# Kernel tuning notes

Hardware: AMD Instinct MI355X
Metric: run time of the kernel (lower is better)

The kernel has to match this reference:

```python
import jax, jax.numpy as jnp
import numpy as np

B, NNZ = 2048, 8
CAT_V, HVEC_V = 10000, 50000
SYN, SEM = 128, 256
HIDDEN, OUT = 1024, 10000


def setup_inputs() -> dict:
    key = jax.random.key(0)
    ks = jax.random.split(key, 12)
    d_onehot = jax.nn.one_hot(jax.random.randint(ks[0], (B,), 0, 7), 7, dtype=jnp.float32)
    cat_b_ix = jax.random.randint(ks[1], (B,), 0, CAT_V)
    hvb_ix = jax.random.randint(ks[2], (B, NNZ), 0, HVEC_V)
    hvf_ix = jax.random.randint(ks[3], (B, NNZ), 0, HVEC_V)
    hvb_top = jax.random.normal(ks[4], (B, SEM), dtype=jnp.float32)
    hvf_top = jax.random.normal(ks[5], (B, SEM), dtype=jnp.float32)
    cat_embeds = jax.random.normal(ks[6], (CAT_V, SYN), dtype=jnp.float32) * 0.02
    hvec_embeds = jax.random.normal(ks[7], (HVEC_V, SEM), dtype=jnp.float32) * 0.02
    in_dim = 7 + SYN + 2 * SEM
    W1 = jax.random.normal(ks[8], (HIDDEN, in_dim), dtype=jnp.float32) / np.sqrt(in_dim)
    b1 = jnp.zeros((HIDDEN,), dtype=jnp.float32)
    W2 = jax.random.normal(ks[9], (OUT, HIDDEN), dtype=jnp.float32) / np.sqrt(HIDDEN)
    b2 = jnp.zeros((OUT,), dtype=jnp.float32)
    return {"d_onehot": d_onehot, "cat_b_ix": cat_b_ix, "hvb_ix": hvb_ix,
            "hvf_ix": hvf_ix, "hvb_top": hvb_top, "hvf_top": hvf_top,
            "cat_embeds": cat_embeds, "hvec_embeds": hvec_embeds,
            "W1": W1, "b1": b1, "W2": W2, "b2": b2}


def _multi_hot(ix, vocab):
    # set-to-1 semantics: duplicates within a row still yield 1 (matches torch loop)
    rows = jnp.arange(ix.shape[0])[:, None]
    return jnp.zeros((ix.shape[0], vocab), dtype=jnp.float32).at[rows, ix].set(1.0)


def reference(d_onehot, cat_b_ix, hvb_ix, hvf_ix, hvb_top, hvf_top,
              cat_embeds, hvec_embeds, W1, b1, W2, b2):
    cat_b_embed = cat_embeds[cat_b_ix]                      # (B, SYN)
    hvb_mat = _multi_hot(hvb_ix, hvec_embeds.shape[0])      # (B, HVEC_V)
    hvf_mat = _multi_hot(hvf_ix, hvec_embeds.shape[0])
    hvb_embed = hvb_mat @ hvec_embeds + hvb_top             # (B, SEM)
    hvf_embed = hvf_mat @ hvec_embeds + hvf_top
    x = jnp.concatenate([cat_b_embed, hvb_embed, hvf_embed, d_onehot], axis=1)
    x = jax.nn.relu(x @ W1.T + b1)
    x = x @ W2.T + b2
    return jax.nn.log_softmax(x, axis=1)
```

## Files before the change

kernel.cpp:

```cpp
#include <hip/hip_runtime.h>

#define B_      2048
#define SYN     128
#define SEM     256
#define IN_DIM  647
#define K1      704
#define HIDDEN  1024
#define OUT_N   10000
#define NNZ     8

typedef __bf16 bf16x8 __attribute__((ext_vector_type(8)));
typedef float  f32x4  __attribute__((ext_vector_type(4)));
typedef __attribute__((address_space(3))) const unsigned short* lds_cp;

__device__ __forceinline__ unsigned short f2b(float v) {
    __bf16 b = (__bf16)v;
    return __builtin_bit_cast(unsigned short, b);
}
__device__ __forceinline__ float b2f(unsigned short u) {
    unsigned v = ((unsigned)u) << 16;
    return __builtin_bit_cast(float, v);
}

__global__ __launch_bounds__(256) void build_x(
    const float* __restrict__ d_onehot,
    const int*   __restrict__ cat_ix,
    const int*   __restrict__ hvb_ix,
    const int*   __restrict__ hvf_ix,
    const float* __restrict__ hvb_top,
    const float* __restrict__ hvf_top,
    const float* __restrict__ cat_embeds,
    const float* __restrict__ hvec_embeds,
    unsigned short* __restrict__ xb)
{
    const int b = blockIdx.x, t = threadIdx.x;
    unsigned short* xrow = xb + (size_t)b * K1;

    if (t < SYN) {
        int c = cat_ix[b];
        xrow[t] = f2b(cat_embeds[(size_t)c * SYN + t]);
    }
    {
        int ix[NNZ];
        #pragma unroll
        for (int j = 0; j < NNZ; ++j) ix[j] = hvb_ix[b * NNZ + j];
        float s = hvb_top[(size_t)b * SEM + t];
        #pragma unroll
        for (int j = 0; j < NNZ; ++j) {
            bool dup = false;
            for (int k2 = 0; k2 < j; ++k2) dup = dup || (ix[j] == ix[k2]);
            if (!dup) s += hvec_embeds[(size_t)ix[j] * SEM + t];
        }
        xrow[SYN + t] = f2b(s);
    }
    {
        int ix[NNZ];
        #pragma unroll
        for (int j = 0; j < NNZ; ++j) ix[j] = hvf_ix[b * NNZ + j];
        float s = hvf_top[(size_t)b * SEM + t];
        #pragma unroll
        for (int j = 0; j < NNZ; ++j) {
            bool dup = false;
            for (int k2 = 0; k2 < j; ++k2) dup = dup || (ix[j] == ix[k2]);
            if (!dup) s += hvec_embeds[(size_t)ix[j] * SEM + t];
        }
        xrow[SYN + SEM + t] = f2b(s);
    }
    if (t < 7)       xrow[640 + t] = f2b(d_onehot[b * 7 + t]);
    else if (t < 64) xrow[640 + t] = 0;
}

__global__ void cvt_w1(const float* __restrict__ W1, unsigned short* __restrict__ W1b) {
    int idx = blockIdx.x * 256 + threadIdx.x;
    if (idx >= HIDDEN * K1) return;
    int r = idx / K1, c = idx - r * K1;
    W1b[idx] = f2b(c < IN_DIM ? W1[r * IN_DIM + c] : 0.f);
}

__global__ __launch_bounds__(256) void cvt_w2(const float* __restrict__ W2,
                                              unsigned short* __restrict__ W2b) {
    size_t i = (size_t)blockIdx.x * 256 + threadIdx.x;
    if (i >= (size_t)OUT_N * HIDDEN / 8) return;
    const float4* src = (const float4*)(W2 + i * 8);
    float4 a = src[0], b = src[1];
    ushort u[8] = { f2b(a.x), f2b(a.y), f2b(a.z), f2b(a.w),
                    f2b(b.x), f2b(b.y), f2b(b.z), f2b(b.w) };
    *(uint4*)(W2b + i * 8) = *(const uint4*)u;
}

template<int NI, int MODE>
__global__ __launch_bounds__(256) void gemm_rt(
    const unsigned short* __restrict__ A,
    const unsigned short* __restrict__ Bm,
    const float* __restrict__ bias,
    void* __restrict__ outp,
    int K, int nt, int ncols, int nbm1, int nm)
{
    constexpr int BN    = 32 * NI;
    constexpr int NB_CH = NI / 2;
    __shared__ __align__(16) unsigned short lds_a[4][128 * 32];
    __shared__ __align__(16) unsigned short lds_b[4][BN * 32];

    const int tid = threadIdx.x;
    const int wv = tid >> 6, ln = tid & 63;
    const int wr = wv >> 1, wc = wv & 1;
    const int lr = ln & 15, lh = ln >> 4;

    const int g   = gridDim.x;
    const int nw  = (blockIdx.x & 7) * (g >> 3) + (blockIdx.x >> 3);
    const int mt  = nw % nm, ntile = nw / nm;
    const int m0  = mt * 128, n0 = ntile * BN;

    const unsigned short* srcA[2];
    const unsigned short* srcB[NB_CH];
    #pragma unroll
    for (int i = 0; i < 2; ++i) {
        int c = tid + i * 256;
        int row = c >> 2, colL = (((c & 3) ^ ((c >> 3) & 3)) << 3);
        srcA[i] = A + (size_t)(m0 + row) * K + colL;
    }
    #pragma unroll
    for (int j = 0; j < NB_CH; ++j) {
        int c = tid + j * 256;
        int row = c >> 2, colL = (((c & 3) ^ ((c >> 3) & 3)) << 3);
        int gr = n0 + row; if (gr > nbm1) gr = nbm1;
        srcB[j] = Bm + (size_t)gr * K + colL;
    }

    auto stage = [&](int buf, int kt) {
        #pragma unroll
        for (int i = 0; i < 2; ++i)
            __builtin_amdgcn_global_load_lds(
                (__attribute__((address_space(1))) const void*)(srcA[i] + kt),
                (__attribute__((address_space(3))) void*)&lds_a[buf][(tid + i * 256) * 8], 16, 0, 0);
        #pragma unroll
        for (int j = 0; j < NB_CH; ++j)
            __builtin_amdgcn_global_load_lds(
                (__attribute__((address_space(1))) const void*)(srcB[j] + kt),
                (__attribute__((address_space(3))) void*)&lds_b[buf][(tid + j * 256) * 8], 16, 0, 0);
    };

    int a_off[4], b_off[NI];
    #pragma unroll
    for (int mi = 0; mi < 4; ++mi) {
        int row = wr * 64 + mi * 16 + lr;
        a_off[mi] = (row * 64 + lh * 16) ^ (((row >> 1) & 3) << 4);
    }
    #pragma unroll
    for (int ni = 0; ni < NI; ++ni) {
        int row = wc * 16 * NI + ni * 16 + lr;
        b_off[ni] = (row * 64 + lh * 16) ^ (((row >> 1) & 3) << 4);
    }

    f32x4 acc[4][NI];
    {
        f32x4 z = {0.f, 0.f, 0.f, 0.f};
        #pragma unroll
        for (int i = 0; i < 4; ++i)
            #pragma unroll
            for (int j = 0; j < NI; ++j) acc[i][j] = z;
    }

    stage(0, 0);
    stage(1, 32);
    if constexpr (NI == 4) asm volatile("s_waitcnt vmcnt(4)" ::: "memory");
    else                   asm volatile("s_waitcnt vmcnt(3)" ::: "memory");
    __builtin_amdgcn_s_barrier();
    asm volatile("" ::: "memory");

    for (int t = 0; t < nt; ++t) {
        const int cur = t & 3, pre = (t + 2) & 3;
        int tp = t + 2; if (tp > nt - 1) tp = nt - 1;

        bf16x8 af[4], bfv[NI];
        lds_cp pa = (lds_cp)&lds_a[cur][0];
        lds_cp pb = (lds_cp)&lds_b[cur][0];
        #pragma unroll
        for (int mi = 0; mi < 4; ++mi) {
            unsigned ad = (unsigned)(unsigned long long)pa + a_off[mi];
            asm volatile("ds_read_b128 %0, %1" : "=v"(af[mi]) : "v"(ad));
        }
        #pragma unroll
        for (int ni = 0; ni < NI; ++ni) {
            unsigned ad = (unsigned)(unsigned long long)pb + b_off[ni];
            asm volatile("ds_read_b128 %0, %1" : "=v"(bfv[ni]) : "v"(ad));
        }

        stage(pre, tp * 32);

        asm volatile("s_waitcnt lgkmcnt(0)" ::: "memory");
        __builtin_amdgcn_sched_barrier(0);

        __builtin_amdgcn_s_setprio(1);
        #pragma unroll
        for (int mi = 0; mi < 4; ++mi)
            #pragma unroll
            for (int ni = 0; ni < NI; ++ni)
                acc[mi][ni] = __builtin_amdgcn_mfma_f32_16x16x32_bf16(af[mi], bfv[ni], acc[mi][ni], 0, 0, 0);
        __builtin_amdgcn_s_setprio(0);

        if constexpr (NI == 4) asm volatile("s_waitcnt vmcnt(4)" ::: "memory");
        else                   asm volatile("s_waitcnt vmcnt(3)" ::: "memory");
        __builtin_amdgcn_s_barrier();
        asm volatile("" ::: "memory");
    }

    #pragma unroll
    for (int mi = 0; mi < 4; ++mi) {
        int row = m0 + wr * 64 + mi * 16 + lh * 4;
        #pragma unroll
        for (int ni = 0; ni < NI; ++ni) {
            int col = n0 + wc * 16 * NI + ni * 16 + lr;
            if (col < ncols) {
                float bb = bias[col];
                if (MODE == 0) {
                    unsigned short* H = (unsigned short*)outp;
                    #pragma unroll
                    for (int r = 0; r < 4; ++r)
                        H[(size_t)(row + r) * ncols + col] = f2b(fmaxf(acc[mi][ni][r] + bb, 0.f));
                } else if (MODE == 1) {
                    unsigned short* H = (unsigned short*)outp;
                    #pragma unroll
                    for (int r = 0; r < 4; ++r)
                        H[(size_t)(row + r) * ncols + col] = f2b(acc[mi][ni][r] + bb);
                } else {
                    float* O = (float*)outp;
                    #pragma unroll
                    for (int r = 0; r < 4; ++r)
                        O[(size_t)(row + r) * ncols + col] = acc[mi][ni][r] + bb;
                }
            }
        }
    }
}

__global__ __launch_bounds__(256) void lsm_b(const unsigned short* __restrict__ lg,
                                             float* __restrict__ out) {
    __shared__ __align__(16) float rowbuf[OUT_N];
    __shared__ float red[8];
    const int t = threadIdx.x, wv = t >> 6, ln = t & 63;
    const unsigned short* l = lg + (size_t)blockIdx.x * OUT_N;
    float* o = out + (size_t)blockIdx.x * OUT_N;

    float mx = -3.4e38f;
    for (int i = t; i < OUT_N / 8; i += 256) {
        uint4 v = ((const uint4*)l)[i];
        float f[8];
        unsigned w[4] = {v.x, v.y, v.z, v.w};
        #pragma unroll
        for (int j = 0; j < 4; ++j) {
            f[2*j]   = __builtin_bit_cast(float, w[j] << 16);
            f[2*j+1] = __builtin_bit_cast(float, w[j] & 0xffff0000u);
        }
        #pragma unroll
        for (int j = 0; j < 8; ++j) {
            rowbuf[i * 8 + j] = f[j];
            mx = fmaxf(mx, f[j]);
        }
    }
    #pragma unroll
    for (int off = 32; off > 0; off >>= 1) mx = fmaxf(mx, __shfl_xor(mx, off, 64));
    if (ln == 0) red[wv] = mx;
    __syncthreads();
    float m4 = fmaxf(fmaxf(red[0], red[1]), fmaxf(red[2], red[3]));

    float s = 0.f;
    for (int i = t; i < OUT_N; i += 256) s += __expf(rowbuf[i] - m4);
    #pragma unroll
    for (int off = 32; off > 0; off >>= 1) s += __shfl_xor(s, off, 64);
    if (ln == 0) red[4 + wv] = s;
    __syncthreads();
    float lz = m4 + logf(red[4] + red[5] + red[6] + red[7]);

    for (int i = t; i < OUT_N / 4; i += 256) {
        float4 v = { rowbuf[i*4] - lz, rowbuf[i*4+1] - lz,
                     rowbuf[i*4+2] - lz, rowbuf[i*4+3] - lz };
        ((float4*)o)[i] = v;
    }
}

__global__ __launch_bounds__(256) void lsm_f(float* __restrict__ out) {
    __shared__ __align__(16) float rowbuf[OUT_N];
    __shared__ float red[8];
    const int t = threadIdx.x, wv = t >> 6, ln = t & 63;
    float* o = out + (size_t)blockIdx.x * OUT_N;

    float mx = -3.4e38f;
    for (int i = t; i < OUT_N / 4; i += 256) {
        float4 v = ((const float4*)o)[i];
        rowbuf[i*4] = v.x; rowbuf[i*4+1] = v.y; rowbuf[i*4+2] = v.z; rowbuf[i*4+3] = v.w;
        mx = fmaxf(fmaxf(mx, fmaxf(v.x, v.y)), fmaxf(v.z, v.w));
    }
    #pragma unroll
    for (int off = 32; off > 0; off >>= 1) mx = fmaxf(mx, __shfl_xor(mx, off, 64));
    if (ln == 0) red[wv] = mx;
    __syncthreads();
    float m4 = fmaxf(fmaxf(red[0], red[1]), fmaxf(red[2], red[3]));

    float s = 0.f;
    for (int i = t; i < OUT_N; i += 256) s += __expf(rowbuf[i] - m4);
    #pragma unroll
    for (int off = 32; off > 0; off >>= 1) s += __shfl_xor(s, off, 64);
    if (ln == 0) red[4 + wv] = s;
    __syncthreads();
    float lz = m4 + logf(red[4] + red[5] + red[6] + red[7]);

    for (int i = t; i < OUT_N / 4; i += 256) {
        float4 v = { rowbuf[i*4] - lz, rowbuf[i*4+1] - lz,
                     rowbuf[i*4+2] - lz, rowbuf[i*4+3] - lz };
        ((float4*)o)[i] = v;
    }
}

extern "C" void kernel_launch(void* const* d_in, const int* in_sizes, int n_in,
                              void* d_out, int out_size, void* d_ws, size_t ws_size,
                              hipStream_t stream) {
    const float* d_onehot    = (const float*)d_in[0];
    const int*   cat_ix      = (const int*)  d_in[1];
    const int*   hvb_ix      = (const int*)  d_in[2];
    const int*   hvf_ix      = (const int*)  d_in[3];
    const float* hvb_top     = (const float*)d_in[4];
    const float* hvf_top     = (const float*)d_in[5];
    const float* cat_embeds  = (const float*)d_in[6];
    const float* hvec_embeds = (const float*)d_in[7];
    const float* W1          = (const float*)d_in[8];
    const float* b1          = (const float*)d_in[9];
    const float* W2          = (const float*)d_in[10];
    const float* b2          = (const float*)d_in[11];
    float* out = (float*)d_out;

    unsigned short* xb  = (unsigned short*)d_ws;
    unsigned short* W1b = xb  + (size_t)B_ * K1;
    unsigned short* hB  = W1b + (size_t)HIDDEN * K1;
    unsigned short* W2b = hB  + (size_t)B_ * HIDDEN;
    unsigned short* lg  = W2b + (size_t)OUT_N * HIDDEN;
    const size_t need = ((size_t)B_*K1 + (size_t)HIDDEN*K1 + (size_t)B_*HIDDEN
                         + (size_t)OUT_N*HIDDEN + (size_t)B_*OUT_N) * 2;
    const bool bf16_logits = (ws_size >= need);

    cvt_w1<<<dim3((HIDDEN * K1 + 255) / 256), dim3(256), 0, stream>>>(W1, W1b);
    cvt_w2<<<dim3((OUT_N * HIDDEN / 8 + 255) / 256), dim3(256), 0, stream>>>(W2, W2b);
    build_x<<<dim3(B_), dim3(256), 0, stream>>>(d_onehot, cat_ix, hvb_ix, hvf_ix,
                                                hvb_top, hvf_top, cat_embeds, hvec_embeds, xb);
    gemm_rt<2, 0><<<dim3(256), dim3(256), 0, stream>>>(
        xb, W1b, b1, (void*)hB, K1, K1 / 32, HIDDEN, HIDDEN - 1, 16);
    if (bf16_logits) {
        gemm_rt<4, 1><<<dim3(16 * 79), dim3(256), 0, stream>>>(
            hB, W2b, b2, (void*)lg, HIDDEN, HIDDEN / 32, OUT_N, OUT_N - 1, 16);
        lsm_b<<<dim3(B_), dim3(256), 0, stream>>>(lg, out);
    } else {
        gemm_rt<4, 2><<<dim3(16 * 79), dim3(256), 0, stream>>>(
            hB, W2b, b2, (void*)out, HIDDEN, HIDDEN / 32, OUT_N, OUT_N - 1, 16);
        lsm_f<<<dim3(B_), dim3(256), 0, stream>>>(out);
    }
}
```

Measured before the change: 119.2 us.

## Fuse prep kernels and double-buffer GEMM fragments with deeper prefetch

Merges the W1/W2 bf16 conversion and input-row building into a single prep launch, removing two kernel launches and gaps. Restructures the GEMM main loop to ping-pong register fragments so LDS reads for the next tile overlap MFMAs of the current one, and prefetches three tiles ahead instead of two. Uses partial lgkmcnt waits; increases register pressure and assumes an even tile count.

New measurement: 116.3 us. 2.5% less time.

```diff
diff --git a/kernel.cpp b/kernel.cpp
--- a/kernel.cpp
+++ b/kernel.cpp
@@ -17,12 +17,12 @@
     __bf16 b = (__bf16)v;
     return __builtin_bit_cast(unsigned short, b);
 }
-__device__ __forceinline__ float b2f(unsigned short u) {
-    unsigned v = ((unsigned)u) << 16;
-    return __builtin_bit_cast(float, v);
-}
-
-__global__ __launch_bounds__(256) void build_x(
+
+#define NB_W1 2816
+#define NB_W2 5000
+__global__ __launch_bounds__(256) void prep(
+    const float* __restrict__ W1,  unsigned short* __restrict__ W1b,
+    const float* __restrict__ W2,  unsigned short* __restrict__ W2b,
     const float* __restrict__ d_onehot,
     const int*   __restrict__ cat_ix,
     const int*   __restrict__ hvb_ix,
@@ -33,9 +33,24 @@
     const float* __restrict__ hvec_embeds,
     unsigned short* __restrict__ xb)
 {
-    const int b = blockIdx.x, t = threadIdx.x;
+    const int bb = blockIdx.x, t = threadIdx.x;
+    if (bb < NB_W1) {
+        int idx = bb * 256 + t;
+        int r = idx / K1, c = idx - r * K1;
+        W1b[idx] = f2b(c < IN_DIM ? W1[r * IN_DIM + c] : 0.f);
+        return;
+    }
+    if (bb < NB_W1 + NB_W2) {
+        size_t i = (size_t)(bb - NB_W1) * 256 + t;
+        const float4* src = (const float4*)(W2 + i * 8);
+        float4 a = src[0], b = src[1];
+        ushort u[8] = { f2b(a.x), f2b(a.y), f2b(a.z), f2b(a.w),
+                        f2b(b.x), f2b(b.y), f2b(b.z), f2b(b.w) };
+        *(uint4*)(W2b + i * 8) = *(const uint4*)u;
+        return;
+    }
+    const int b = bb - (NB_W1 + NB_W2);
     unsigned short* xrow = xb + (size_t)b * K1;
-
     if (t < SYN) {
         int c = cat_ix[b];
         xrow[t] = f2b(cat_embeds[(size_t)c * SYN + t]);
@@ -68,24 +83,6 @@
     }
     if (t < 7)       xrow[640 + t] = f2b(d_onehot[b * 7 + t]);
     else if (t < 64) xrow[640 + t] = 0;
-}
-
-__global__ void cvt_w1(const float* __restrict__ W1, unsigned short* __restrict__ W1b) {
-    int idx = blockIdx.x * 256 + threadIdx.x;
-    if (idx >= HIDDEN * K1) return;
-    int r = idx / K1, c = idx - r * K1;
-    W1b[idx] = f2b(c < IN_DIM ? W1[r * IN_DIM + c] : 0.f);
-}
-
-__global__ __launch_bounds__(256) void cvt_w2(const float* __restrict__ W2,
-                                              unsigned short* __restrict__ W2b) {
-    size_t i = (size_t)blockIdx.x * 256 + threadIdx.x;
-    if (i >= (size_t)OUT_N * HIDDEN / 8) return;
-    const float4* src = (const float4*)(W2 + i * 8);
-    float4 a = src[0], b = src[1];
-    ushort u[8] = { f2b(a.x), f2b(a.y), f2b(a.z), f2b(a.w),
-                    f2b(b.x), f2b(b.y), f2b(b.z), f2b(b.w) };
-    *(uint4*)(W2b + i * 8) = *(const uint4*)u;
 }
 
 template<int NI, int MODE>
@@ -161,20 +158,9 @@
             for (int j = 0; j < NI; ++j) acc[i][j] = z;
     }
 
-    stage(0, 0);
-    stage(1, 32);
-    if constexpr (NI == 4) asm volatile("s_waitcnt vmcnt(4)" ::: "memory");
-    else                   asm volatile("s_waitcnt vmcnt(3)" ::: "memory");
-    __builtin_amdgcn_s_barrier();
-    asm volatile("" ::: "memory");
-
-    for (int t = 0; t < nt; ++t) {
-        const int cur = t & 3, pre = (t + 2) & 3;
-        int tp = t + 2; if (tp > nt - 1) tp = nt - 1;
-
-        bf16x8 af[4], bfv[NI];
-        lds_cp pa = (lds_cp)&lds_a[cur][0];
-        lds_cp pb = (lds_cp)&lds_b[cur][0];
+    auto frag_read = [&](bf16x8 (&af)[4], bf16x8 (&bfv)[NI], int buf) {
+        lds_cp pa = (lds_cp)&lds_a[buf][0];
+        lds_cp pb = (lds_cp)&lds_b[buf][0];
         #pragma unroll
         for (int mi = 0; mi < 4; ++mi) {
             unsigned ad = (unsigned)(unsigned long long)pa + a_off[mi];
@@ -185,24 +171,43 @@
             unsigned ad = (unsigned)(unsigned long long)pb + b_off[ni];
             asm volatile("ds_read_b128 %0, %1" : "=v"(bfv[ni]) : "v"(ad));
         }
-
-        stage(pre, tp * 32);
-
-        asm volatile("s_waitcnt lgkmcnt(0)" ::: "memory");
-        __builtin_amdgcn_sched_barrier(0);
-
-        __builtin_amdgcn_s_setprio(1);
+    };
+    auto do_mfma = [&](bf16x8 (&af)[4], bf16x8 (&bfv)[NI]) {
         #pragma unroll
         for (int mi = 0; mi < 4; ++mi)
             #pragma unroll
             for (int ni = 0; ni < NI; ++ni)
                 acc[mi][ni] = __builtin_amdgcn_mfma_f32_16x16x32_bf16(af[mi], bfv[ni], acc[mi][ni], 0, 0, 0);
+    };
+    auto do_part = [&](bf16x8 (&rA)[4], bf16x8 (&rB)[NI],
+                       bf16x8 (&mA)[4], bf16x8 (&mB)[NI], int p) {
+        frag_read(rA, rB, (p + 1) & 3);
+        int tp = p + 3; if (tp > nt - 1) tp = nt - 1;
+        stage((p + 3) & 3, tp * 32);
+        if constexpr (NI == 4) asm volatile("s_waitcnt lgkmcnt(8)" ::: "memory");
+        else                   asm volatile("s_waitcnt lgkmcnt(6)" ::: "memory");
+        __builtin_amdgcn_sched_barrier(0);
+        __builtin_amdgcn_s_setprio(1);
+        do_mfma(mA, mB);
         __builtin_amdgcn_s_setprio(0);
-
         if constexpr (NI == 4) asm volatile("s_waitcnt vmcnt(4)" ::: "memory");
         else                   asm volatile("s_waitcnt vmcnt(3)" ::: "memory");
         __builtin_amdgcn_s_barrier();
-        asm volatile("" ::: "memory");
+    };
+
+    stage(0, 0);
+    stage(1, 32);
+    stage(2, 64);
+    if constexpr (NI == 4) asm volatile("s_waitcnt vmcnt(4)" ::: "memory");
+    else                   asm volatile("s_waitcnt vmcnt(3)" ::: "memory");
+    __builtin_amdgcn_s_barrier();
+
+    bf16x8 afX[4], bfX[NI], afY[4], bfY[NI];
+    frag_read(afX, bfX, 0);
+
+    for (int t = 0; t < nt; t += 2) {
+        do_part(afY, bfY, afX, bfX, t);
+        do_part(afX, bfX, afY, bfY, t + 1);
     }
 
     #pragma unroll
@@ -338,10 +343,9 @@
                          + (size_t)OUT_N*HIDDEN + (size_t)B_*OUT_N) * 2;
     const bool bf16_logits = (ws_size >= need);
 
-    cvt_w1<<<dim3((HIDDEN * K1 + 255) / 256), dim3(256), 0, stream>>>(W1, W1b);
-    cvt_w2<<<dim3((OUT_N * HIDDEN / 8 + 255) / 256), dim3(256), 0, stream>>>(W2, W2b);
-    build_x<<<dim3(B_), dim3(256), 0, stream>>>(d_onehot, cat_ix, hvb_ix, hvf_ix,
-                                                hvb_top, hvf_top, cat_embeds, hvec_embeds, xb);
+    prep<<<dim3(NB_W1 + NB_W2 + B_), dim3(256), 0, stream>>>(
+        W1, W1b, W2, W2b, d_onehot, cat_ix, hvb_ix, hvf_ix,
+        hvb_top, hvf_top, cat_embeds, hvec_embeds, xb);
     gemm_rt<2, 0><<<dim3(256), dim3(256), 0, stream>>>(
         xb, W1b, b1, (void*)hB, K1, K1 / 32, HIDDEN, HIDDEN - 1, 16);
     if (bf16_logits) {
```
